# Optimization experiments

Hardware: AMD Instinct MI355X
Metric: run time of the kernel (lower is better)

Reference implementation:

```python
import jax, jax.numpy as jnp
import numpy as np

TOP_K = 2
EPS = 1e-6


def setup_inputs() -> dict:
    key = jax.random.key(0)
    ks = jax.random.split(key, 8)
    B, S, D, E = 4, 2048, 2048, 8
    sd = 1.0 / np.sqrt(D)
    return {
        "x": jax.random.normal(ks[0], (B, S, D), dtype=jnp.float32),
        "Wr": jax.random.normal(ks[1], (D, E), dtype=jnp.float32) * sd,
        "br": jnp.zeros((E,), dtype=jnp.float32),
        "We": jax.random.normal(ks[2], (E, D, D), dtype=jnp.float32) * sd,
        "be": jnp.zeros((E, D), dtype=jnp.float32),
        "Wo": jax.random.normal(ks[3], (D, D), dtype=jnp.float32) * sd,
        "bo": jnp.zeros((D,), dtype=jnp.float32),
        "norm_w": jnp.ones((D,), dtype=jnp.float32),
    }


def reference(x, Wr, br, We, be, Wo, bo, norm_w):
    B, S, D = x.shape
    xf = x.reshape(-1, D)  # [T, D]
    # Router + top-k gating (softmax over the k selected logits, as in source)
    logits = xf @ Wr + br                      # [T, E]
    vals, idx = jax.lax.top_k(logits, TOP_K)   # [T, K]
    gates = jax.nn.softmax(vals, axis=-1)      # [T, K]
    # Expert FFN: Linear -> SiLU (dropout=0 -> identity). Dense over all experts,
    # then gather the top-k outputs per token.
    all_out = jax.nn.silu(jnp.einsum('td,edf->tef', xf, We) + be)  # [T, E, D]
    picked = jnp.take_along_axis(all_out, idx[:, :, None], axis=1)  # [T, K, D]
    combined = jnp.sum(gates[:, :, None] * picked, axis=1)          # [T, D]
    out = combined @ Wo + bo
    y = xf + out
    rms = jnp.sqrt(jnp.mean(y * y, axis=-1, keepdims=True) + EPS)
    return (norm_w * (y / rms)).reshape(B, S, D)
```

## Files before the change

kernel.cpp:

```cpp
#include <hip/hip_runtime.h>
#include <hip/hip_bf16.h>
#include <stdint.h>

typedef __bf16 bf16;
typedef __bf16 bf16x4 __attribute__((ext_vector_type(4)));
typedef __bf16 bf16x8 __attribute__((ext_vector_type(8)));
typedef float floatx4 __attribute__((ext_vector_type(4)));

#define T_TOK 8192
#define DIM 2048
#define NE 8
#define MAX_CHUNKS 136

__device__ inline void gld_lds16(const bf16* g, bf16* l) {
  __builtin_amdgcn_global_load_lds(
      (const __attribute__((address_space(1))) uint32_t*)g,
      (__attribute__((address_space(3))) uint32_t*)l, 16, 0, 0);
}

__global__ __launch_bounds__(256) void transpose_convert(
    const float* __restrict__ in, bf16* __restrict__ out) {
  __shared__ float tile[32][33];
  const int tx = threadIdx.x & 31;
  const int ty = threadIdx.x >> 5;
  const int n0 = blockIdx.x * 32;
  const int k0 = blockIdx.y * 32;
  const size_t base = (size_t)blockIdx.z * DIM * DIM;
  const float* src = in + base;
  bf16* dst = out + base;
#pragma unroll
  for (int i = 0; i < 32; i += 8)
    tile[ty + i][tx] = src[(size_t)(k0 + ty + i) * DIM + n0 + tx];
  __syncthreads();
#pragma unroll
  for (int i = 0; i < 32; i += 8)
    dst[(size_t)(n0 + ty + i) * DIM + k0 + tx] = (bf16)tile[tx][ty + i];
}

__global__ __launch_bounds__(256) void router_kernel(
    const float* __restrict__ x, const float* __restrict__ Wr,
    const float* __restrict__ br, int* __restrict__ cnt,
    int* __restrict__ aid_list, float* __restrict__ gate_list,
    bf16* __restrict__ xb) {
  const int t = blockIdx.x;
  const int tid = threadIdx.x;
  const float* xr = x + (size_t)t * DIM;
  bf16* xbr = xb + (size_t)t * DIM;
  float acc[8];
#pragma unroll
  for (int e = 0; e < 8; ++e) acc[e] = 0.f;
#pragma unroll
  for (int h = 0; h < 2; ++h) {
    const int d0 = tid * 4 + h * 1024;
    float4 xv = *(const float4*)&xr[d0];
    bf16x4 xc;
    xc[0] = (bf16)xv.x; xc[1] = (bf16)xv.y; xc[2] = (bf16)xv.z; xc[3] = (bf16)xv.w;
    *(bf16x4*)&xbr[d0] = xc;
    const float* wp = &Wr[(size_t)d0 * NE];
    float xe[4] = {xv.x, xv.y, xv.z, xv.w};
#pragma unroll
    for (int q = 0; q < 4; ++q) {
      float4 w0 = *(const float4*)&wp[q * 8];
      float4 w1 = *(const float4*)&wp[q * 8 + 4];
      acc[0] += xe[q] * w0.x; acc[1] += xe[q] * w0.y;
      acc[2] += xe[q] * w0.z; acc[3] += xe[q] * w0.w;
      acc[4] += xe[q] * w1.x; acc[5] += xe[q] * w1.y;
      acc[6] += xe[q] * w1.z; acc[7] += xe[q] * w1.w;
    }
  }
#pragma unroll
  for (int e = 0; e < 8; ++e) {
#pragma unroll
    for (int off = 32; off > 0; off >>= 1) acc[e] += __shfl_down(acc[e], off, 64);
  }
  __shared__ float red[4][8];
  const int lane = tid & 63, wid = tid >> 6;
  if (lane == 0) {
#pragma unroll
    for (int e = 0; e < 8; ++e) red[wid][e] = acc[e];
  }
  __syncthreads();
  if (tid == 0) {
    float lg[8];
#pragma unroll
    for (int e = 0; e < 8; ++e)
      lg[e] = red[0][e] + red[1][e] + red[2][e] + red[3][e] + br[e];
    int i0 = 0;
#pragma unroll
    for (int e = 1; e < 8; ++e) if (lg[e] > lg[i0]) i0 = e;
    int i1 = (i0 == 0) ? 1 : 0;
#pragma unroll
    for (int e = 0; e < 8; ++e)
      if (e != i0 && lg[e] > lg[i1]) i1 = e;
    const float g0 = 1.f / (1.f + expf(lg[i1] - lg[i0]));
    const float g1 = 1.f - g0;
    int p0 = atomicAdd(&cnt[i0], 1);
    aid_list[i0 * T_TOK + p0] = t * 2;
    gate_list[i0 * T_TOK + p0] = g0;
    int p1 = atomicAdd(&cnt[i1], 1);
    aid_list[i1 * T_TOK + p1] = t * 2 + 1;
    gate_list[i1 * T_TOK + p1] = g1;
  }
}

__global__ void build_chunks(const int* __restrict__ cnt, int2* __restrict__ chunks,
                             int* __restrict__ nchunks) {
  if (threadIdx.x == 0 && blockIdx.x == 0) {
    int tot = 0;
#pragma unroll
    for (int e = 0; e < NE; ++e) {
      const int ne = cnt[e];
      for (int m0 = 0; m0 < ne; m0 += 128) chunks[tot++] = make_int2(e, m0);
    }
    *nchunks = tot;
  }
}


__global__ __launch_bounds__(256, 2) void expert_gemm(
    const bf16* __restrict__ xb, const bf16* __restrict__ Wt,
    const float* __restrict__ be, const int* __restrict__ cnt,
    const int* __restrict__ aid_list, const float* __restrict__ gate_list,
    const int2* __restrict__ chunks, const int* __restrict__ nchunks,
    bf16* __restrict__ aout) {
  const int cid = blockIdx.x;
  if (cid >= *nchunks) return;
  const int2 ch = chunks[cid];
  const int e = ch.x;
  const int m0 = ch.y;
  const int ne = cnt[e];
  const int n0 = blockIdx.y * 128;
  const int tid = threadIdx.x;

  __shared__ bf16 As[128][64];
  __shared__ bf16 Bs[128][64];
  __shared__ int aidS[128];
  __shared__ float gateS[128];

  if (tid < 128) {
    const int idx = m0 + tid;
    aidS[tid] = (idx < ne) ? aid_list[e * T_TOK + idx] : 0;
    gateS[tid] = (idx < ne) ? gate_list[e * T_TOK + idx] : 0.f;
  }
  __syncthreads();

  const int r0 = tid >> 3;
  const int kq = (((tid & 7) ^ (r0 & 7))) * 8;
  const bf16* wbase = Wt + (size_t)e * DIM * DIM;
  const bf16* ap[4];
  const bf16* bp[4];
#pragma unroll
  for (int h = 0; h < 4; ++h) {
    const int r = r0 + 32 * h;
    ap[h] = xb + (size_t)(aidS[r] >> 1) * DIM + kq;
    bp[h] = wbase + (size_t)(n0 + r) * DIM + kq;
  }
  bf16* const asF = &As[0][0];
  bf16* const bsF = &Bs[0][0];

  const int lane = tid & 63, wid = tid >> 6;
  const int wr = (wid >> 1) * 64, wc = (wid & 1) * 64;
  const int quad = lane >> 4, l15 = lane & 15;

  floatx4 acc[4][4];
#pragma unroll
  for (int i = 0; i < 4; ++i)
#pragma unroll
    for (int j = 0; j < 4; ++j) acc[i][j] = (floatx4){0.f, 0.f, 0.f, 0.f};

  int aoff[2][4], boff[2][4];
#pragma unroll
  for (int s = 0; s < 2; ++s) {
    const int kb = s * 4 + quad;
#pragma unroll
    for (int i = 0; i < 4; ++i) {
      const int mi = wr + i * 16 + l15;
      aoff[s][i] = mi * 64 + ((kb ^ (mi & 7)) * 8);
      const int nj = wc + i * 16 + l15;
      boff[s][i] = nj * 64 + ((kb ^ (nj & 7)) * 8);
    }
  }

  for (int k0 = 0; k0 < DIM; k0 += 64) {
#pragma unroll
    for (int h = 0; h < 4; ++h) {
      gld_lds16(bp[h] + k0, bsF + ((size_t)tid + 256 * h) * 8);
      gld_lds16(ap[h] + k0, asF + ((size_t)tid + 256 * h) * 8);
    }
    __syncthreads();

#pragma unroll
    for (int s = 0; s < 2; ++s) {
      bf16x8 af[4], bfr[4];
#pragma unroll
      for (int i = 0; i < 4; ++i) af[i] = *(const bf16x8*)&asF[aoff[s][i]];
#pragma unroll
      for (int j = 0; j < 4; ++j) bfr[j] = *(const bf16x8*)&bsF[boff[s][j]];
#pragma unroll
      for (int i = 0; i < 4; ++i)
#pragma unroll
        for (int j = 0; j < 4; ++j)
          acc[i][j] = __builtin_amdgcn_mfma_f32_16x16x32_bf16(af[i], bfr[j], acc[i][j], 0, 0, 0);
    }
    __syncthreads();
  }

#pragma unroll
  for (int j = 0; j < 4; ++j) {
    const int col = n0 + wc + j * 16 + l15;
    const float bev = be[e * DIM + col];
#pragma unroll
    for (int i = 0; i < 4; ++i) {
#pragma unroll
      for (int r = 0; r < 4; ++r) {
        const int rl = wr + i * 16 + quad * 4 + r;
        if (m0 + rl < ne) {
          float v = acc[i][j][r] + bev;
          v = v / (1.f + __expf(-v));
          v *= gateS[rl];
          aout[(size_t)aidS[rl] * DIM + col] = (bf16)v;
        }
      }
    }
  }
}

__global__ __launch_bounds__(256) void combine_kernel(
    const bf16* __restrict__ aout, bf16* __restrict__ hcomb) {
  const size_t i = ((size_t)blockIdx.x * 256 + threadIdx.x) * 8;
  const size_t row = i >> 11;
  const size_t d = i & 2047;
  const bf16* a0 = aout + (row << 12) + d;
  bf16x8 u0 = *(const bf16x8*)a0;
  bf16x8 u1 = *(const bf16x8*)(a0 + DIM);
  bf16x8 s;
#pragma unroll
  for (int q = 0; q < 8; ++q) s[q] = (bf16)((float)u0[q] + (float)u1[q]);
  *(bf16x8*)&hcomb[i] = s;
}

__global__ __launch_bounds__(256, 2) void proj_gemm(
    const bf16* __restrict__ hcomb, const bf16* __restrict__ Wot,
    const float* __restrict__ bo, const float* __restrict__ x,
    float* __restrict__ y) {
  const int m0 = blockIdx.x * 128;
  const int n0 = blockIdx.y * 128;
  const int tid = threadIdx.x;

  __shared__ bf16 As[128][64];
  __shared__ bf16 Bs[128][64];

  const int r0 = tid >> 3;
  const int kq = (((tid & 7) ^ (r0 & 7))) * 8;
  const bf16* ap[4];
  const bf16* bp[4];
#pragma unroll
  for (int h = 0; h < 4; ++h) {
    const int r = r0 + 32 * h;
    ap[h] = hcomb + (size_t)(m0 + r) * DIM + kq;
    bp[h] = Wot + (size_t)(n0 + r) * DIM + kq;
  }
  bf16* const asF = &As[0][0];
  bf16* const bsF = &Bs[0][0];

  const int lane = tid & 63, wid = tid >> 6;
  const int wr = (wid >> 1) * 64, wc = (wid & 1) * 64;
  const int quad = lane >> 4, l15 = lane & 15;

  floatx4 acc[4][4];
#pragma unroll
  for (int i = 0; i < 4; ++i)
#pragma unroll
    for (int j = 0; j < 4; ++j) acc[i][j] = (floatx4){0.f, 0.f, 0.f, 0.f};

  int aoff[2][4], boff[2][4];
#pragma unroll
  for (int s = 0; s < 2; ++s) {
    const int kb = s * 4 + quad;
#pragma unroll
    for (int i = 0; i < 4; ++i) {
      const int mi = wr + i * 16 + l15;
      aoff[s][i] = mi * 64 + ((kb ^ (mi & 7)) * 8);
      const int nj = wc + i * 16 + l15;
      boff[s][i] = nj * 64 + ((kb ^ (nj & 7)) * 8);
    }
  }

  for (int k0 = 0; k0 < DIM; k0 += 64) {
#pragma unroll
    for (int h = 0; h < 4; ++h) {
      gld_lds16(bp[h] + k0, bsF + ((size_t)tid + 256 * h) * 8);
      gld_lds16(ap[h] + k0, asF + ((size_t)tid + 256 * h) * 8);
    }
    __syncthreads();

#pragma unroll
    for (int s = 0; s < 2; ++s) {
      bf16x8 af[4], bfr[4];
#pragma unroll
      for (int i = 0; i < 4; ++i) af[i] = *(const bf16x8*)&asF[aoff[s][i]];
#pragma unroll
      for (int j = 0; j < 4; ++j) bfr[j] = *(const bf16x8*)&bsF[boff[s][j]];
#pragma unroll
      for (int i = 0; i < 4; ++i)
#pragma unroll
        for (int j = 0; j < 4; ++j)
          acc[i][j] = __builtin_amdgcn_mfma_f32_16x16x32_bf16(af[i], bfr[j], acc[i][j], 0, 0, 0);
    }
    __syncthreads();
  }

#pragma unroll
  for (int j = 0; j < 4; ++j) {
    const int col = n0 + wc + j * 16 + l15;
    const float bov = bo[col];
#pragma unroll
    for (int i = 0; i < 4; ++i) {
#pragma unroll
      for (int r = 0; r < 4; ++r) {
        const int rl = wr + i * 16 + quad * 4 + r;
        const size_t o = (size_t)(m0 + rl) * DIM + col;
        y[o] = acc[i][j][r] + bov + x[o];
      }
    }
  }
}

__global__ __launch_bounds__(256) void rmsnorm_kernel(
    float* __restrict__ y, const float* __restrict__ w) {
  const int row = blockIdx.x;
  const int tid = threadIdx.x;
  float* yr = y + (size_t)row * DIM;
  float4 v0 = ((const float4*)yr)[tid];
  float4 v1 = ((const float4*)yr)[tid + 256];
  float ss = v0.x * v0.x + v0.y * v0.y + v0.z * v0.z + v0.w * v0.w +
             v1.x * v1.x + v1.y * v1.y + v1.z * v1.z + v1.w * v1.w;
#pragma unroll
  for (int off = 32; off > 0; off >>= 1) ss += __shfl_down(ss, off, 64);
  __shared__ float s4[4];
  const int lane = tid & 63, wid = tid >> 6;
  if (lane == 0) s4[wid] = ss;
  __syncthreads();
  const float tot = s4[0] + s4[1] + s4[2] + s4[3];
  const float r = rsqrtf(tot / (float)DIM + 1e-6f);
  float4 w0 = ((const float4*)w)[tid];
  float4 w1 = ((const float4*)w)[tid + 256];
  float4 o0 = make_float4(v0.x * r * w0.x, v0.y * r * w0.y, v0.z * r * w0.z, v0.w * r * w0.w);
  float4 o1 = make_float4(v1.x * r * w1.x, v1.y * r * w1.y, v1.z * r * w1.z, v1.w * r * w1.w);
  ((float4*)yr)[tid] = o0;
  ((float4*)yr)[tid + 256] = o1;
}

extern "C" void kernel_launch(void* const* d_in, const int* in_sizes, int n_in,
                              void* d_out, int out_size, void* d_ws, size_t ws_size,
                              hipStream_t stream) {
  const float* x  = (const float*)d_in[0];
  const float* Wr = (const float*)d_in[1];
  const float* br = (const float*)d_in[2];
  const float* We = (const float*)d_in[3];
  const float* be = (const float*)d_in[4];
  const float* Wo = (const float*)d_in[5];
  const float* bo = (const float*)d_in[6];
  const float* nw = (const float*)d_in[7];
  float* out = (float*)d_out;

  uint8_t* ws = (uint8_t*)d_ws;
  size_t off = 0;
  auto carve = [&](size_t bytes) -> void* {
    void* p = ws + off;
    off += (bytes + 255) & ~(size_t)255;
    return p;
  };
  int*   cnt       = (int*)carve(NE * sizeof(int));
  int*   aid_list  = (int*)carve((size_t)NE * T_TOK * sizeof(int));
  float* gate_list = (float*)carve((size_t)NE * T_TOK * sizeof(float));
  int2*  chunks    = (int2*)carve(MAX_CHUNKS * sizeof(int2));
  int*   nchunks   = (int*)carve(sizeof(int));
  bf16*  We_t      = (bf16*)carve((size_t)NE * DIM * DIM * sizeof(bf16));
  bf16*  Wo_t      = (bf16*)carve((size_t)DIM * DIM * sizeof(bf16));
  bf16*  aoutb     = (bf16*)carve((size_t)T_TOK * 2 * DIM * sizeof(bf16));
  bf16*  xb        = (bf16*)carve((size_t)T_TOK * DIM * sizeof(bf16));
  bf16*  hcomb     = We_t;
  (void)ws_size; (void)in_sizes; (void)n_in; (void)out_size;

  hipMemsetAsync(cnt, 0, NE * sizeof(int), stream);
  transpose_convert<<<dim3(DIM / 32, DIM / 32, NE), 256, 0, stream>>>(We, We_t);
  transpose_convert<<<dim3(DIM / 32, DIM / 32, 1), 256, 0, stream>>>(Wo, Wo_t);
  router_kernel<<<T_TOK, 256, 0, stream>>>(x, Wr, br, cnt, aid_list, gate_list, xb);
  build_chunks<<<1, 64, 0, stream>>>(cnt, chunks, nchunks);
  expert_gemm<<<dim3(MAX_CHUNKS, DIM / 128), 256, 0, stream>>>(
      xb, We_t, be, cnt, aid_list, gate_list, chunks, nchunks, aoutb);
  combine_kernel<<<(T_TOK * DIM / 8) / 256, 256, 0, stream>>>(aoutb, hcomb);
  proj_gemm<<<dim3(T_TOK / 128, DIM / 128), 256, 0, stream>>>(hcomb, Wo_t, bo, x, out);
  rmsnorm_kernel<<<T_TOK, 256, 0, stream>>>(out, nw);
}
```

Before: 840.6 us.

## Use 256x256 double-buffered GEMM tiles with interleaved prefetch and block swizzle

Expert and projection GEMMs move from 128x128 tiles with 256 threads to 256x256 tiles with 512 threads and a double-buffered LDS. The next K-tile's global-to-LDS loads are spread between the MFMA phases, and setprio is raised around the MFMA bursts. Block indices are remapped so the eight N-column blocks of one M chunk are spread across the grid. The aim is to raise operand reuse, hide load latency and cut barrier stalls, at the cost of 128KB of LDS per block, higher register pressure and coarser padding waste for experts whose token count is not a multiple of 256.

Result: slower. 890.6 us (+6.0%).

```diff
diff --git a/kernel.cpp b/kernel.cpp
--- a/kernel.cpp
+++ b/kernel.cpp
@@ -10,7 +10,9 @@
 #define T_TOK 8192
 #define DIM 2048
 #define NE 8
-#define MAX_CHUNKS 136
+#define NT (DIM / 64)
+#define MAX_CHUNKS 72
+#define PROJ_CIDS 32
 
 __device__ inline void gld_lds16(const bf16* g, bf16* l) {
   __builtin_amdgcn_global_load_lds(
@@ -110,34 +112,70 @@
 #pragma unroll
     for (int e = 0; e < NE; ++e) {
       const int ne = cnt[e];
-      for (int m0 = 0; m0 < ne; m0 += 128) chunks[tot++] = make_int2(e, m0);
+      for (int m0 = 0; m0 < ne; m0 += 256) chunks[tot++] = make_int2(e, m0);
     }
     *nchunks = tot;
   }
 }
 
 
-__global__ __launch_bounds__(256, 2) void expert_gemm(
+#define GEMM_TILE_PHASES(STAGE_EXPR)                                          \
+  {                                                                           \
+    bf16x8 af[4], bfr[4];                                                     \
+_Pragma("unroll")                                                             \
+    for (int s = 0; s < 2; ++s) {                                             \
+      const int xo = s ? x1 : x0;                                             \
+_Pragma("unroll")                                                             \
+      for (int mh = 0; mh < 2; ++mh) {                                        \
+        if (mh == 0) {                                                        \
+_Pragma("unroll")                                                             \
+          for (int j = 0; j < 4; ++j)                                         \
+            bfr[j] = *(const bf16x8*)&bsF[bbase + xo + j * 1024];             \
+        }                                                                     \
+_Pragma("unroll")                                                             \
+        for (int i = 0; i < 4; ++i)                                           \
+          af[i] = *(const bf16x8*)&asF[abase + xo + (mh * 4 + i) * 1024];     \
+        const int ph = s * 2 + mh;                                            \
+        if ((STAGE_EXPR) && ph < 3) {                                         \
+          const int h = ph + 1;                                               \
+          gld_lds16(ap[h] + kn, asN + (size_t)(tid + 512 * h) * 8);           \
+          gld_lds16(bp[h] + kn, bsN + (size_t)(tid + 512 * h) * 8);           \
+        }                                                                     \
+        __builtin_amdgcn_s_setprio(1);                                        \
+_Pragma("unroll")                                                             \
+        for (int i = 0; i < 4; ++i)                                           \
+_Pragma("unroll")                                                             \
+          for (int j = 0; j < 4; ++j)                                         \
+            acc[mh * 4 + i][j] = __builtin_amdgcn_mfma_f32_16x16x32_bf16(     \
+                af[i], bfr[j], acc[mh * 4 + i][j], 0, 0, 0);                  \
+        __builtin_amdgcn_s_setprio(0);                                        \
+      }                                                                       \
+    }                                                                         \
+  }
+
+__global__ __launch_bounds__(512, 2) void expert_gemm(
     const bf16* __restrict__ xb, const bf16* __restrict__ Wt,
     const float* __restrict__ be, const int* __restrict__ cnt,
     const int* __restrict__ aid_list, const float* __restrict__ gate_list,
     const int2* __restrict__ chunks, const int* __restrict__ nchunks,
     bf16* __restrict__ aout) {
-  const int cid = blockIdx.x;
+  int wg = blockIdx.x;
+  wg = (wg & 7) * MAX_CHUNKS + (wg >> 3);
+  const int cid = wg >> 3;
   if (cid >= *nchunks) return;
   const int2 ch = chunks[cid];
   const int e = ch.x;
   const int m0 = ch.y;
   const int ne = cnt[e];
-  const int n0 = blockIdx.y * 128;
+  const int n0 = (wg & 7) * 256;
   const int tid = threadIdx.x;
 
-  __shared__ bf16 As[128][64];
-  __shared__ bf16 Bs[128][64];
-  __shared__ int aidS[128];
-  __shared__ float gateS[128];
-
-  if (tid < 128) {
+  __shared__ bf16 As[2][256 * 64];
+  __shared__ bf16 Bs[2][256 * 64];
+  __shared__ int aidS[256];
+  __shared__ float gateS[256];
+
+  if (tid < 256) {
     const int idx = m0 + tid;
     aidS[tid] = (idx < ne) ? aid_list[e * T_TOK + idx] : 0;
     gateS[tid] = (idx < ne) ? gate_list[e * T_TOK + idx] : 0.f;
@@ -145,75 +183,71 @@
   __syncthreads();
 
   const int r0 = tid >> 3;
-  const int kq = (((tid & 7) ^ (r0 & 7))) * 8;
+  const int kq = ((tid & 7) ^ (r0 & 7)) * 8;
   const bf16* wbase = Wt + (size_t)e * DIM * DIM;
   const bf16* ap[4];
   const bf16* bp[4];
 #pragma unroll
   for (int h = 0; h < 4; ++h) {
-    const int r = r0 + 32 * h;
+    const int r = r0 + 64 * h;
     ap[h] = xb + (size_t)(aidS[r] >> 1) * DIM + kq;
     bp[h] = wbase + (size_t)(n0 + r) * DIM + kq;
   }
-  bf16* const asF = &As[0][0];
-  bf16* const bsF = &Bs[0][0];
-
-  const int lane = tid & 63, wid = tid >> 6;
-  const int wr = (wid >> 1) * 64, wc = (wid & 1) * 64;
+
+  const int lane = tid & 63, w = tid >> 6;
+  const int wm = w >> 2, wn = w & 3;
   const int quad = lane >> 4, l15 = lane & 15;
-
-  floatx4 acc[4][4];
-#pragma unroll
-  for (int i = 0; i < 4; ++i)
+  const int x0 = ((quad) ^ (l15 & 7)) * 8;
+  const int x1 = ((quad + 4) ^ (l15 & 7)) * 8;
+  const int abase = (wm * 128 + l15) * 64;
+  const int bbase = (wn * 64 + l15) * 64;
+
+  floatx4 acc[8][4];
+#pragma unroll
+  for (int i = 0; i < 8; ++i)
 #pragma unroll
     for (int j = 0; j < 4; ++j) acc[i][j] = (floatx4){0.f, 0.f, 0.f, 0.f};
 
-  int aoff[2][4], boff[2][4];
-#pragma unroll
-  for (int s = 0; s < 2; ++s) {
-    const int kb = s * 4 + quad;
-#pragma unroll
-    for (int i = 0; i < 4; ++i) {
-      const int mi = wr + i * 16 + l15;
-      aoff[s][i] = mi * 64 + ((kb ^ (mi & 7)) * 8);
-      const int nj = wc + i * 16 + l15;
-      boff[s][i] = nj * 64 + ((kb ^ (nj & 7)) * 8);
-    }
-  }
-
-  for (int k0 = 0; k0 < DIM; k0 += 64) {
-#pragma unroll
-    for (int h = 0; h < 4; ++h) {
-      gld_lds16(bp[h] + k0, bsF + ((size_t)tid + 256 * h) * 8);
-      gld_lds16(ap[h] + k0, asF + ((size_t)tid + 256 * h) * 8);
-    }
-    __syncthreads();
-
-#pragma unroll
-    for (int s = 0; s < 2; ++s) {
-      bf16x8 af[4], bfr[4];
-#pragma unroll
-      for (int i = 0; i < 4; ++i) af[i] = *(const bf16x8*)&asF[aoff[s][i]];
-#pragma unroll
-      for (int j = 0; j < 4; ++j) bfr[j] = *(const bf16x8*)&bsF[boff[s][j]];
-#pragma unroll
-      for (int i = 0; i < 4; ++i)
-#pragma unroll
-        for (int j = 0; j < 4; ++j)
-          acc[i][j] = __builtin_amdgcn_mfma_f32_16x16x32_bf16(af[i], bfr[j], acc[i][j], 0, 0, 0);
-    }
-    __syncthreads();
+#pragma unroll
+  for (int h = 0; h < 4; ++h) {
+    gld_lds16(ap[h], &As[0][(size_t)(tid + 512 * h) * 8]);
+    gld_lds16(bp[h], &Bs[0][(size_t)(tid + 512 * h) * 8]);
+  }
+
+  int p = 0;
+  for (int t = 0; t < NT; ++t) {
+    const bf16* asF = &As[p][0];
+    const bf16* bsF = &Bs[p][0];
+    bf16* asN = &As[p ^ 1][0];
+    bf16* bsN = &Bs[p ^ 1][0];
+    const int kn = (t + 1) * 64;
+    const bool stage = (t + 1 < NT);
+
+    asm volatile("" ::: "memory");
+    __builtin_amdgcn_s_barrier();
+    if (stage) {
+      gld_lds16(ap[0] + kn, asN + (size_t)tid * 8);
+      gld_lds16(bp[0] + kn, bsN + (size_t)tid * 8);
+      asm volatile("s_waitcnt vmcnt(2)" ::: "memory");
+    } else {
+      asm volatile("s_waitcnt vmcnt(0)" ::: "memory");
+    }
+    __builtin_amdgcn_s_barrier();
+    asm volatile("" ::: "memory");
+
+    GEMM_TILE_PHASES(stage)
+    p ^= 1;
   }
 
 #pragma unroll
   for (int j = 0; j < 4; ++j) {
-    const int col = n0 + wc + j * 16 + l15;
+    const int col = n0 + wn * 64 + j * 16 + l15;
     const float bev = be[e * DIM + col];
 #pragma unroll
-    for (int i = 0; i < 4; ++i) {
+    for (int i = 0; i < 8; ++i) {
 #pragma unroll
       for (int r = 0; r < 4; ++r) {
-        const int rl = wr + i * 16 + quad * 4 + r;
+        const int rl = wm * 128 + i * 16 + quad * 4 + r;
         if (m0 + rl < ne) {
           float v = acc[i][j][r] + bev;
           v = v / (1.f + __expf(-v));
@@ -239,86 +273,84 @@
   *(bf16x8*)&hcomb[i] = s;
 }
 
-__global__ __launch_bounds__(256, 2) void proj_gemm(
+__global__ __launch_bounds__(512, 2) void proj_gemm(
     const bf16* __restrict__ hcomb, const bf16* __restrict__ Wot,
     const float* __restrict__ bo, const float* __restrict__ x,
     float* __restrict__ y) {
-  const int m0 = blockIdx.x * 128;
-  const int n0 = blockIdx.y * 128;
+  int wg = blockIdx.x;
+  wg = (wg & 7) * PROJ_CIDS + (wg >> 3);
+  const int m0 = (wg >> 3) * 256;
+  const int n0 = (wg & 7) * 256;
   const int tid = threadIdx.x;
 
-  __shared__ bf16 As[128][64];
-  __shared__ bf16 Bs[128][64];
+  __shared__ bf16 As[2][256 * 64];
+  __shared__ bf16 Bs[2][256 * 64];
 
   const int r0 = tid >> 3;
-  const int kq = (((tid & 7) ^ (r0 & 7))) * 8;
+  const int kq = ((tid & 7) ^ (r0 & 7)) * 8;
   const bf16* ap[4];
   const bf16* bp[4];
 #pragma unroll
   for (int h = 0; h < 4; ++h) {
-    const int r = r0 + 32 * h;
+    const int r = r0 + 64 * h;
     ap[h] = hcomb + (size_t)(m0 + r) * DIM + kq;
     bp[h] = Wot + (size_t)(n0 + r) * DIM + kq;
   }
-  bf16* const asF = &As[0][0];
-  bf16* const bsF = &Bs[0][0];
-
-  const int lane = tid & 63, wid = tid >> 6;
-  const int wr = (wid >> 1) * 64, wc = (wid & 1) * 64;
+
+  const int lane = tid & 63, w = tid >> 6;
+  const int wm = w >> 2, wn = w & 3;
   const int quad = lane >> 4, l15 = lane & 15;
-
-  floatx4 acc[4][4];
-#pragma unroll
-  for (int i = 0; i < 4; ++i)
+  const int x0 = ((quad) ^ (l15 & 7)) * 8;
+  const int x1 = ((quad + 4) ^ (l15 & 7)) * 8;
+  const int abase = (wm * 128 + l15) * 64;
+  const int bbase = (wn * 64 + l15) * 64;
+
+  floatx4 acc[8][4];
+#pragma unroll
+  for (int i = 0; i < 8; ++i)
 #pragma unroll
     for (int j = 0; j < 4; ++j) acc[i][j] = (floatx4){0.f, 0.f, 0.f, 0.f};
 
-  int aoff[2][4], boff[2][4];
-#pragma unroll
-  for (int s = 0; s < 2; ++s) {
-    const int kb = s * 4 + quad;
-#pragma unroll
-    for (int i = 0; i < 4; ++i) {
-      const int mi = wr + i * 16 + l15;
-      aoff[s][i] = mi * 64 + ((kb ^ (mi & 7)) * 8);
-      const int nj = wc + i * 16 + l15;
-      boff[s][i] = nj * 64 + ((kb ^ (nj & 7)) * 8);
-    }
-  }
-
-  for (int k0 = 0; k0 < DIM; k0 += 64) {
-#pragma unroll
-    for (int h = 0; h < 4; ++h) {
-      gld_lds16(bp[h] + k0, bsF + ((size_t)tid + 256 * h) * 8);
-      gld_lds16(ap[h] + k0, asF + ((size_t)tid + 256 * h) * 8);
-    }
-    __syncthreads();
-
-#pragma unroll
-    for (int s = 0; s < 2; ++s) {
-      bf16x8 af[4], bfr[4];
-#pragma unroll
-      for (int i = 0; i < 4; ++i) af[i] = *(const bf16x8*)&asF[aoff[s][i]];
-#pragma unroll
-      for (int j = 0; j < 4; ++j) bfr[j] = *(const bf16x8*)&bsF[boff[s][j]];
-#pragma unroll
-      for (int i = 0; i < 4; ++i)
-#pragma unroll
-        for (int j = 0; j < 4; ++j)
-          acc[i][j] = __builtin_amdgcn_mfma_f32_16x16x32_bf16(af[i], bfr[j], acc[i][j], 0, 0, 0);
-    }
-    __syncthreads();
+#pragma unroll
+  for (int h = 0; h < 4; ++h) {
+    gld_lds16(ap[h], &As[0][(size_t)(tid + 512 * h) * 8]);
+    gld_lds16(bp[h], &Bs[0][(size_t)(tid + 512 * h) * 8]);
+  }
+
+  int p = 0;
+  for (int t = 0; t < NT; ++t) {
+    const bf16* asF = &As[p][0];
+    const bf16* bsF = &Bs[p][0];
+    bf16* asN = &As[p ^ 1][0];
+    bf16* bsN = &Bs[p ^ 1][0];
+    const int kn = (t + 1) * 64;
+    const bool stage = (t + 1 < NT);
+
+    asm volatile("" ::: "memory");
+    __builtin_amdgcn_s_barrier();
+    if (stage) {
+      gld_lds16(ap[0] + kn, asN + (size_t)tid * 8);
+      gld_lds16(bp[0] + kn, bsN + (size_t)tid * 8);
+      asm volatile("s_waitcnt vmcnt(2)" ::: "memory");
+    } else {
+      asm volatile("s_waitcnt vmcnt(0)" ::: "memory");
+    }
+    __builtin_amdgcn_s_barrier();
+    asm volatile("" ::: "memory");
+
+    GEMM_TILE_PHASES(stage)
+    p ^= 1;
   }
 
 #pragma unroll
   for (int j = 0; j < 4; ++j) {
-    const int col = n0 + wc + j * 16 + l15;
+    const int col = n0 + wn * 64 + j * 16 + l15;
     const float bov = bo[col];
 #pragma unroll
-    for (int i = 0; i < 4; ++i) {
+    for (int i = 0; i < 8; ++i) {
 #pragma unroll
       for (int r = 0; r < 4; ++r) {
-        const int rl = wr + i * 16 + quad * 4 + r;
+        const int rl = wm * 128 + i * 16 + quad * 4 + r;
         const size_t o = (size_t)(m0 + rl) * DIM + col;
         y[o] = acc[i][j][r] + bov + x[o];
       }
@@ -388,9 +420,9 @@
   transpose_convert<<<dim3(DIM / 32, DIM / 32, 1), 256, 0, stream>>>(Wo, Wo_t);
   router_kernel<<<T_TOK, 256, 0, stream>>>(x, Wr, br, cnt, aid_list, gate_list, xb);
   build_chunks<<<1, 64, 0, stream>>>(cnt, chunks, nchunks);
-  expert_gemm<<<dim3(MAX_CHUNKS, DIM / 128), 256, 0, stream>>>(
+  expert_gemm<<<dim3(MAX_CHUNKS * 8), 512, 0, stream>>>(
       xb, We_t, be, cnt, aid_list, gate_list, chunks, nchunks, aoutb);
   combine_kernel<<<(T_TOK * DIM / 8) / 256, 256, 0, stream>>>(aoutb, hcomb);
-  proj_gemm<<<dim3(T_TOK / 128, DIM / 128), 256, 0, stream>>>(hcomb, Wo_t, bo, x, out);
+  proj_gemm<<<dim3(PROJ_CIDS * 8), 512, 0, stream>>>(hcomb, Wo_t, bo, x, out);
   rmsnorm_kernel<<<T_TOK, 256, 0, stream>>>(out, nw);
 }
```

## Double-buffer GEMM K-loop and fuse top-2 combine into projection A-load

Applied to the files above, without the earlier changes.

Both expert and projection GEMMs switch to BK=32 double-buffered LDS tiles, prefetching the next tile while MFMAs run on the current one, with occupancy hint raised to 4 blocks per CU. The separate combine kernel is removed; proj_gemm now loads both per-token expert outputs, sums them in registers and writes the sum to LDS, saving a full intermediate write/read pass. Grids are flattened to 1D with N-tiles fastest, so consecutive blocks share the same A rows. Trade-offs are twice as many barriers per K and register-path A loads in proj_gemm instead of direct-to-LDS loads.

New measurement: 863.8 us. 1.03x slower.

```diff
diff --git a/kernel.cpp b/kernel.cpp
--- a/kernel.cpp
+++ b/kernel.cpp
@@ -10,6 +10,10 @@
 #define T_TOK 8192
 #define DIM 2048
 #define NE 8
+#define BM 128
+#define BN 128
+#define BK 32
+#define NTIL (DIM / BK)
 #define MAX_CHUNKS 136
 
 __device__ inline void gld_lds16(const bf16* g, bf16* l) {
@@ -110,57 +114,62 @@
 #pragma unroll
     for (int e = 0; e < NE; ++e) {
       const int ne = cnt[e];
-      for (int m0 = 0; m0 < ne; m0 += 128) chunks[tot++] = make_int2(e, m0);
+      for (int m0 = 0; m0 < ne; m0 += BM) chunks[tot++] = make_int2(e, m0);
     }
     *nchunks = tot;
   }
 }
 
 
-__global__ __launch_bounds__(256, 2) void expert_gemm(
+__global__ __launch_bounds__(256, 4) void expert_gemm(
     const bf16* __restrict__ xb, const bf16* __restrict__ Wt,
     const float* __restrict__ be, const int* __restrict__ cnt,
     const int* __restrict__ aid_list, const float* __restrict__ gate_list,
     const int2* __restrict__ chunks, const int* __restrict__ nchunks,
     bf16* __restrict__ aout) {
-  const int cid = blockIdx.x;
+  const int cid = blockIdx.x >> 4;
   if (cid >= *nchunks) return;
   const int2 ch = chunks[cid];
   const int e = ch.x;
   const int m0 = ch.y;
   const int ne = cnt[e];
-  const int n0 = blockIdx.y * 128;
+  const int n0 = (blockIdx.x & 15) * BN;
   const int tid = threadIdx.x;
 
-  __shared__ bf16 As[128][64];
-  __shared__ bf16 Bs[128][64];
-  __shared__ int aidS[128];
-  __shared__ float gateS[128];
-
-  if (tid < 128) {
+  __shared__ bf16 As[2][BM * BK];
+  __shared__ bf16 Bs[2][BM * BK];
+  __shared__ int aidS[BM];
+  __shared__ float gateS[BM];
+
+  if (tid < BM) {
     const int idx = m0 + tid;
     aidS[tid] = (idx < ne) ? aid_list[e * T_TOK + idx] : 0;
     gateS[tid] = (idx < ne) ? gate_list[e * T_TOK + idx] : 0.f;
   }
   __syncthreads();
 
-  const int r0 = tid >> 3;
-  const int kq = (((tid & 7) ^ (r0 & 7))) * 8;
-  const bf16* wbase = Wt + (size_t)e * DIM * DIM;
-  const bf16* ap[4];
-  const bf16* bp[4];
-#pragma unroll
-  for (int h = 0; h < 4; ++h) {
-    const int r = r0 + 32 * h;
+  const int kq = ((tid & 3) ^ ((tid >> 3) & 3)) * 8;
+  const int r0 = tid >> 2;
+  const bf16* wb = Wt + (size_t)e * DIM * DIM;
+  const bf16* ap[2];
+  const bf16* bp[2];
+#pragma unroll
+  for (int h = 0; h < 2; ++h) {
+    const int r = r0 + 64 * h;
     ap[h] = xb + (size_t)(aidS[r] >> 1) * DIM + kq;
-    bp[h] = wbase + (size_t)(n0 + r) * DIM + kq;
-  }
-  bf16* const asF = &As[0][0];
-  bf16* const bsF = &Bs[0][0];
-
-  const int lane = tid & 63, wid = tid >> 6;
-  const int wr = (wid >> 1) * 64, wc = (wid & 1) * 64;
+    bp[h] = wb + (size_t)(n0 + r) * DIM + kq;
+  }
+
+  const int lane = tid & 63, w = tid >> 6;
+  const int wm = w >> 1, wn = w & 1;
   const int quad = lane >> 4, l15 = lane & 15;
+  const int xo = (quad ^ ((l15 >> 1) & 3)) * 8;
+  int aoff[4], boff[4];
+#pragma unroll
+  for (int i = 0; i < 4; ++i) {
+    aoff[i] = (wm * 64 + i * 16 + l15) * BK + xo;
+    boff[i] = (wn * 64 + i * 16 + l15) * BK + xo;
+  }
 
   floatx4 acc[4][4];
 #pragma unroll
@@ -168,52 +177,51 @@
 #pragma unroll
     for (int j = 0; j < 4; ++j) acc[i][j] = (floatx4){0.f, 0.f, 0.f, 0.f};
 
-  int aoff[2][4], boff[2][4];
-#pragma unroll
-  for (int s = 0; s < 2; ++s) {
-    const int kb = s * 4 + quad;
+  bf16* a_cur = &As[0][0]; bf16* a_nxt = &As[1][0];
+  bf16* b_cur = &Bs[0][0]; bf16* b_nxt = &Bs[1][0];
+
+#pragma unroll
+  for (int h = 0; h < 2; ++h) {
+    gld_lds16(ap[h], a_cur + (tid + 256 * h) * 8);
+    gld_lds16(bp[h], b_cur + (tid + 256 * h) * 8);
+  }
+  asm volatile("s_waitcnt vmcnt(0)" ::: "memory");
+  __builtin_amdgcn_s_barrier();
+
+  for (int t = 0; t < NTIL; ++t) {
+    if (t + 1 < NTIL) {
+      const int kn = (t + 1) * BK;
+#pragma unroll
+      for (int h = 0; h < 2; ++h) {
+        gld_lds16(ap[h] + kn, a_nxt + (tid + 256 * h) * 8);
+        gld_lds16(bp[h] + kn, b_nxt + (tid + 256 * h) * 8);
+      }
+    }
+    bf16x8 af[4];
+#pragma unroll
+    for (int i = 0; i < 4; ++i) af[i] = *(const bf16x8*)&a_cur[aoff[i]];
+#pragma unroll
+    for (int j = 0; j < 4; ++j) {
+      const bf16x8 bfr = *(const bf16x8*)&b_cur[boff[j]];
+#pragma unroll
+      for (int i = 0; i < 4; ++i)
+        acc[i][j] = __builtin_amdgcn_mfma_f32_16x16x32_bf16(af[i], bfr, acc[i][j], 0, 0, 0);
+    }
+    asm volatile("s_waitcnt vmcnt(0)" ::: "memory");
+    __builtin_amdgcn_s_barrier();
+    bf16* tA = a_cur; a_cur = a_nxt; a_nxt = tA;
+    bf16* tB = b_cur; b_cur = b_nxt; b_nxt = tB;
+  }
+
+#pragma unroll
+  for (int j = 0; j < 4; ++j) {
+    const int col = n0 + wn * 64 + j * 16 + l15;
+    const float bev = be[e * DIM + col];
 #pragma unroll
     for (int i = 0; i < 4; ++i) {
-      const int mi = wr + i * 16 + l15;
-      aoff[s][i] = mi * 64 + ((kb ^ (mi & 7)) * 8);
-      const int nj = wc + i * 16 + l15;
-      boff[s][i] = nj * 64 + ((kb ^ (nj & 7)) * 8);
-    }
-  }
-
-  for (int k0 = 0; k0 < DIM; k0 += 64) {
-#pragma unroll
-    for (int h = 0; h < 4; ++h) {
-      gld_lds16(bp[h] + k0, bsF + ((size_t)tid + 256 * h) * 8);
-      gld_lds16(ap[h] + k0, asF + ((size_t)tid + 256 * h) * 8);
-    }
-    __syncthreads();
-
-#pragma unroll
-    for (int s = 0; s < 2; ++s) {
-      bf16x8 af[4], bfr[4];
-#pragma unroll
-      for (int i = 0; i < 4; ++i) af[i] = *(const bf16x8*)&asF[aoff[s][i]];
-#pragma unroll
-      for (int j = 0; j < 4; ++j) bfr[j] = *(const bf16x8*)&bsF[boff[s][j]];
-#pragma unroll
-      for (int i = 0; i < 4; ++i)
-#pragma unroll
-        for (int j = 0; j < 4; ++j)
-          acc[i][j] = __builtin_amdgcn_mfma_f32_16x16x32_bf16(af[i], bfr[j], acc[i][j], 0, 0, 0);
-    }
-    __syncthreads();
-  }
-
-#pragma unroll
-  for (int j = 0; j < 4; ++j) {
-    const int col = n0 + wc + j * 16 + l15;
-    const float bev = be[e * DIM + col];
-#pragma unroll
-    for (int i = 0; i < 4; ++i) {
 #pragma unroll
       for (int r = 0; r < 4; ++r) {
-        const int rl = wr + i * 16 + quad * 4 + r;
+        const int rl = wm * 64 + i * 16 + quad * 4 + r;
         if (m0 + rl < ne) {
           float v = acc[i][j][r] + bev;
           v = v / (1.f + __expf(-v));
@@ -225,47 +233,38 @@
   }
 }
 
-__global__ __launch_bounds__(256) void combine_kernel(
-    const bf16* __restrict__ aout, bf16* __restrict__ hcomb) {
-  const size_t i = ((size_t)blockIdx.x * 256 + threadIdx.x) * 8;
-  const size_t row = i >> 11;
-  const size_t d = i & 2047;
-  const bf16* a0 = aout + (row << 12) + d;
-  bf16x8 u0 = *(const bf16x8*)a0;
-  bf16x8 u1 = *(const bf16x8*)(a0 + DIM);
-  bf16x8 s;
-#pragma unroll
-  for (int q = 0; q < 8; ++q) s[q] = (bf16)((float)u0[q] + (float)u1[q]);
-  *(bf16x8*)&hcomb[i] = s;
-}
-
-__global__ __launch_bounds__(256, 2) void proj_gemm(
-    const bf16* __restrict__ hcomb, const bf16* __restrict__ Wot,
+__global__ __launch_bounds__(256, 4) void proj_gemm(
+    const bf16* __restrict__ aout, const bf16* __restrict__ Wot,
     const float* __restrict__ bo, const float* __restrict__ x,
     float* __restrict__ y) {
-  const int m0 = blockIdx.x * 128;
-  const int n0 = blockIdx.y * 128;
+  const int m0 = (int)(blockIdx.x >> 4) * BM;
+  const int n0 = (int)(blockIdx.x & 15) * BN;
   const int tid = threadIdx.x;
 
-  __shared__ bf16 As[128][64];
-  __shared__ bf16 Bs[128][64];
-
-  const int r0 = tid >> 3;
-  const int kq = (((tid & 7) ^ (r0 & 7))) * 8;
-  const bf16* ap[4];
-  const bf16* bp[4];
-#pragma unroll
-  for (int h = 0; h < 4; ++h) {
-    const int r = r0 + 32 * h;
-    ap[h] = hcomb + (size_t)(m0 + r) * DIM + kq;
+  __shared__ bf16 As[2][BM * BK];
+  __shared__ bf16 Bs[2][BM * BK];
+
+  const int kq = ((tid & 3) ^ ((tid >> 3) & 3)) * 8;
+  const int r0 = tid >> 2;
+  const bf16* a0[2];
+  const bf16* bp[2];
+#pragma unroll
+  for (int h = 0; h < 2; ++h) {
+    const int r = r0 + 64 * h;
+    a0[h] = aout + (size_t)(2 * (m0 + r)) * DIM + kq;
     bp[h] = Wot + (size_t)(n0 + r) * DIM + kq;
   }
-  bf16* const asF = &As[0][0];
-  bf16* const bsF = &Bs[0][0];
-
-  const int lane = tid & 63, wid = tid >> 6;
-  const int wr = (wid >> 1) * 64, wc = (wid & 1) * 64;
+
+  const int lane = tid & 63, w = tid >> 6;
+  const int wm = w >> 1, wn = w & 1;
   const int quad = lane >> 4, l15 = lane & 15;
+  const int xo = (quad ^ ((l15 >> 1) & 3)) * 8;
+  int aoff[4], boff[4];
+#pragma unroll
+  for (int i = 0; i < 4; ++i) {
+    aoff[i] = (wm * 64 + i * 16 + l15) * BK + xo;
+    boff[i] = (wn * 64 + i * 16 + l15) * BK + xo;
+  }
 
   floatx4 acc[4][4];
 #pragma unroll
@@ -273,52 +272,76 @@
 #pragma unroll
     for (int j = 0; j < 4; ++j) acc[i][j] = (floatx4){0.f, 0.f, 0.f, 0.f};
 
-  int aoff[2][4], boff[2][4];
-#pragma unroll
-  for (int s = 0; s < 2; ++s) {
-    const int kb = s * 4 + quad;
+  bf16* a_cur = &As[0][0]; bf16* a_nxt = &As[1][0];
+  bf16* b_cur = &Bs[0][0]; bf16* b_nxt = &Bs[1][0];
+
+  {
+    bf16x8 u[2][2];
+#pragma unroll
+    for (int h = 0; h < 2; ++h) {
+      gld_lds16(bp[h], b_cur + (tid + 256 * h) * 8);
+      u[h][0] = *(const bf16x8*)(a0[h]);
+      u[h][1] = *(const bf16x8*)(a0[h] + DIM);
+    }
+#pragma unroll
+    for (int h = 0; h < 2; ++h) {
+      bf16x8 s;
+#pragma unroll
+      for (int q = 0; q < 8; ++q)
+        s[q] = (bf16)((float)u[h][0][q] + (float)u[h][1][q]);
+      *(bf16x8*)&a_cur[(tid + 256 * h) * 8] = s;
+    }
+  }
+  asm volatile("s_waitcnt vmcnt(0) lgkmcnt(0)" ::: "memory");
+  __builtin_amdgcn_s_barrier();
+
+  for (int t = 0; t < NTIL; ++t) {
+    bf16x8 v[2][2];
+    const bool stage = (t + 1 < NTIL);
+    if (stage) {
+      const int kn = (t + 1) * BK;
+#pragma unroll
+      for (int h = 0; h < 2; ++h) {
+        gld_lds16(bp[h] + kn, b_nxt + (tid + 256 * h) * 8);
+        v[h][0] = *(const bf16x8*)(a0[h] + kn);
+        v[h][1] = *(const bf16x8*)(a0[h] + kn + DIM);
+      }
+    }
+    bf16x8 af[4];
+#pragma unroll
+    for (int i = 0; i < 4; ++i) af[i] = *(const bf16x8*)&a_cur[aoff[i]];
+#pragma unroll
+    for (int j = 0; j < 4; ++j) {
+      const bf16x8 bfr = *(const bf16x8*)&b_cur[boff[j]];
+#pragma unroll
+      for (int i = 0; i < 4; ++i)
+        acc[i][j] = __builtin_amdgcn_mfma_f32_16x16x32_bf16(af[i], bfr, acc[i][j], 0, 0, 0);
+    }
+    if (stage) {
+#pragma unroll
+      for (int h = 0; h < 2; ++h) {
+        bf16x8 s;
+#pragma unroll
+        for (int q = 0; q < 8; ++q)
+          s[q] = (bf16)((float)v[h][0][q] + (float)v[h][1][q]);
+        *(bf16x8*)&a_nxt[(tid + 256 * h) * 8] = s;
+      }
+    }
+    asm volatile("s_waitcnt vmcnt(0) lgkmcnt(0)" ::: "memory");
+    __builtin_amdgcn_s_barrier();
+    bf16* tA = a_cur; a_cur = a_nxt; a_nxt = tA;
+    bf16* tB = b_cur; b_cur = b_nxt; b_nxt = tB;
+  }
+
+#pragma unroll
+  for (int j = 0; j < 4; ++j) {
+    const int col = n0 + wn * 64 + j * 16 + l15;
+    const float bov = bo[col];
 #pragma unroll
     for (int i = 0; i < 4; ++i) {
-      const int mi = wr + i * 16 + l15;
-      aoff[s][i] = mi * 64 + ((kb ^ (mi & 7)) * 8);
-      const int nj = wc + i * 16 + l15;
-      boff[s][i] = nj * 64 + ((kb ^ (nj & 7)) * 8);
-    }
-  }
-
-  for (int k0 = 0; k0 < DIM; k0 += 64) {
-#pragma unroll
-    for (int h = 0; h < 4; ++h) {
-      gld_lds16(bp[h] + k0, bsF + ((size_t)tid + 256 * h) * 8);
-      gld_lds16(ap[h] + k0, asF + ((size_t)tid + 256 * h) * 8);
-    }
-    __syncthreads();
-
-#pragma unroll
-    for (int s = 0; s < 2; ++s) {
-      bf16x8 af[4], bfr[4];
-#pragma unroll
-      for (int i = 0; i < 4; ++i) af[i] = *(const bf16x8*)&asF[aoff[s][i]];
-#pragma unroll
-      for (int j = 0; j < 4; ++j) bfr[j] = *(const bf16x8*)&bsF[boff[s][j]];
-#pragma unroll
-      for (int i = 0; i < 4; ++i)
-#pragma unroll
-        for (int j = 0; j < 4; ++j)
-          acc[i][j] = __builtin_amdgcn_mfma_f32_16x16x32_bf16(af[i], bfr[j], acc[i][j], 0, 0, 0);
-    }
-    __syncthreads();
-  }
-
-#pragma unroll
-  for (int j = 0; j < 4; ++j) {
-    const int col = n0 + wc + j * 16 + l15;
-    const float bov = bo[col];
-#pragma unroll
-    for (int i = 0; i < 4; ++i) {
 #pragma unroll
       for (int r = 0; r < 4; ++r) {
-        const int rl = wr + i * 16 + quad * 4 + r;
+        const int rl = wm * 64 + i * 16 + quad * 4 + r;
         const size_t o = (size_t)(m0 + rl) * DIM + col;
         y[o] = acc[i][j][r] + bov + x[o];
       }
@@ -380,7 +403,6 @@
   bf16*  Wo_t      = (bf16*)carve((size_t)DIM * DIM * sizeof(bf16));
   bf16*  aoutb     = (bf16*)carve((size_t)T_TOK * 2 * DIM * sizeof(bf16));
   bf16*  xb        = (bf16*)carve((size_t)T_TOK * DIM * sizeof(bf16));
-  bf16*  hcomb     = We_t;
   (void)ws_size; (void)in_sizes; (void)n_in; (void)out_size;
 
   hipMemsetAsync(cnt, 0, NE * sizeof(int), stream);
@@ -388,9 +410,8 @@
   transpose_convert<<<dim3(DIM / 32, DIM / 32, 1), 256, 0, stream>>>(Wo, Wo_t);
   router_kernel<<<T_TOK, 256, 0, stream>>>(x, Wr, br, cnt, aid_list, gate_list, xb);
   build_chunks<<<1, 64, 0, stream>>>(cnt, chunks, nchunks);
-  expert_gemm<<<dim3(MAX_CHUNKS, DIM / 128), 256, 0, stream>>>(
+  expert_gemm<<<dim3(MAX_CHUNKS * 16), 256, 0, stream>>>(
       xb, We_t, be, cnt, aid_list, gate_list, chunks, nchunks, aoutb);
-  combine_kernel<<<(T_TOK * DIM / 8) / 256, 256, 0, stream>>>(aoutb, hcomb);
-  proj_gemm<<<dim3(T_TOK / 128, DIM / 128), 256, 0, stream>>>(hcomb, Wo_t, bo, x, out);
+  proj_gemm<<<dim3((T_TOK / BM) * 16), 256, 0, stream>>>(aoutb, Wo_t, bo, x, out);
   rmsnorm_kernel<<<T_TOK, 256, 0, stream>>>(out, nw);
 }
```

## Scatter tokens into expert-grouped buffers and fuse combine into projection GEMM

Applied to the files above, without the earlier changes.

The router now writes each token's bf16 copy directly into per-expert padded row buffers and records an inverse index. The expert GEMM therefore reads contiguous A rows and writes contiguous outputs. The separate combine kernel is removed: the projection GEMM gathers both expert outputs per token through registers, sums them, and stores them to shared memory. Chunk building is computed inline, the cnt memset and the two transposes are merged into one launch, and launch bounds go to 3 blocks per SM. The risks are a per-expert count above EPAD overflowing its buffer, and the loss of the direct global-to-LDS load for the projection A operand.

Result: no change. 853.8 us (+1.6%).

```diff
diff --git a/kernel.cpp b/kernel.cpp
--- a/kernel.cpp
+++ b/kernel.cpp
@@ -10,6 +10,7 @@
 #define T_TOK 8192
 #define DIM 2048
 #define NE 8
+#define EPAD 2560
 #define MAX_CHUNKS 136
 
 __device__ inline void gld_lds16(const bf16* g, bf16* l) {
@@ -19,15 +20,18 @@
 }
 
 __global__ __launch_bounds__(256) void transpose_convert(
-    const float* __restrict__ in, bf16* __restrict__ out) {
+    const float* __restrict__ We, const float* __restrict__ Wo,
+    bf16* __restrict__ We_t, bf16* __restrict__ Wo_t, int* __restrict__ cnt) {
+  const int z = blockIdx.z;
+  if (z == 8 && blockIdx.x == 0 && blockIdx.y == 0 && threadIdx.x < NE)
+    cnt[threadIdx.x] = 0;
+  const float* src = (z < 8) ? We + (size_t)z * DIM * DIM : Wo;
+  bf16* dst = (z < 8) ? We_t + (size_t)z * DIM * DIM : Wo_t;
   __shared__ float tile[32][33];
   const int tx = threadIdx.x & 31;
   const int ty = threadIdx.x >> 5;
   const int n0 = blockIdx.x * 32;
   const int k0 = blockIdx.y * 32;
-  const size_t base = (size_t)blockIdx.z * DIM * DIM;
-  const float* src = in + base;
-  bf16* dst = out + base;
 #pragma unroll
   for (int i = 0; i < 32; i += 8)
     tile[ty + i][tx] = src[(size_t)(k0 + ty + i) * DIM + n0 + tx];
@@ -40,24 +44,21 @@
 __global__ __launch_bounds__(256) void router_kernel(
     const float* __restrict__ x, const float* __restrict__ Wr,
     const float* __restrict__ br, int* __restrict__ cnt,
-    int* __restrict__ aid_list, float* __restrict__ gate_list,
-    bf16* __restrict__ xb) {
+    float* __restrict__ gate_list, int2* __restrict__ inv,
+    bf16* __restrict__ xg) {
   const int t = blockIdx.x;
   const int tid = threadIdx.x;
   const float* xr = x + (size_t)t * DIM;
-  bf16* xbr = xb + (size_t)t * DIM;
+  float4 xv[2];
   float acc[8];
 #pragma unroll
   for (int e = 0; e < 8; ++e) acc[e] = 0.f;
 #pragma unroll
   for (int h = 0; h < 2; ++h) {
     const int d0 = tid * 4 + h * 1024;
-    float4 xv = *(const float4*)&xr[d0];
-    bf16x4 xc;
-    xc[0] = (bf16)xv.x; xc[1] = (bf16)xv.y; xc[2] = (bf16)xv.z; xc[3] = (bf16)xv.w;
-    *(bf16x4*)&xbr[d0] = xc;
+    xv[h] = *(const float4*)&xr[d0];
     const float* wp = &Wr[(size_t)d0 * NE];
-    float xe[4] = {xv.x, xv.y, xv.z, xv.w};
+    float xe[4] = {xv[h].x, xv[h].y, xv[h].z, xv[h].w};
 #pragma unroll
     for (int q = 0; q < 4; ++q) {
       float4 w0 = *(const float4*)&wp[q * 8];
@@ -74,6 +75,7 @@
     for (int off = 32; off > 0; off >>= 1) acc[e] += __shfl_down(acc[e], off, 64);
   }
   __shared__ float red[4][8];
+  __shared__ int sRow[2];
   const int lane = tid & 63, wid = tid >> 6;
   if (lane == 0) {
 #pragma unroll
@@ -94,72 +96,73 @@
       if (e != i0 && lg[e] > lg[i1]) i1 = e;
     const float g0 = 1.f / (1.f + expf(lg[i1] - lg[i0]));
     const float g1 = 1.f - g0;
-    int p0 = atomicAdd(&cnt[i0], 1);
-    aid_list[i0 * T_TOK + p0] = t * 2;
+    const int p0 = atomicAdd(&cnt[i0], 1);
+    const int p1 = atomicAdd(&cnt[i1], 1);
     gate_list[i0 * T_TOK + p0] = g0;
-    int p1 = atomicAdd(&cnt[i1], 1);
-    aid_list[i1 * T_TOK + p1] = t * 2 + 1;
     gate_list[i1 * T_TOK + p1] = g1;
-  }
-}
-
-__global__ void build_chunks(const int* __restrict__ cnt, int2* __restrict__ chunks,
-                             int* __restrict__ nchunks) {
-  if (threadIdx.x == 0 && blockIdx.x == 0) {
-    int tot = 0;
-#pragma unroll
-    for (int e = 0; e < NE; ++e) {
-      const int ne = cnt[e];
-      for (int m0 = 0; m0 < ne; m0 += 128) chunks[tot++] = make_int2(e, m0);
-    }
-    *nchunks = tot;
-  }
-}
-
-
-__global__ __launch_bounds__(256, 2) void expert_gemm(
-    const bf16* __restrict__ xb, const bf16* __restrict__ Wt,
+    sRow[0] = i0 * EPAD + p0;
+    sRow[1] = i1 * EPAD + p1;
+    inv[t] = make_int2(sRow[0], sRow[1]);
+  }
+  __syncthreads();
+  const size_t r0 = (size_t)sRow[0] * DIM;
+  const size_t r1 = (size_t)sRow[1] * DIM;
+#pragma unroll
+  for (int h = 0; h < 2; ++h) {
+    const int d0 = tid * 4 + h * 1024;
+    bf16x4 xc;
+    xc[0] = (bf16)xv[h].x; xc[1] = (bf16)xv[h].y;
+    xc[2] = (bf16)xv[h].z; xc[3] = (bf16)xv[h].w;
+    *(bf16x4*)&xg[r0 + d0] = xc;
+    *(bf16x4*)&xg[r1 + d0] = xc;
+  }
+}
+
+
+__global__ __launch_bounds__(256, 3) void expert_gemm(
+    const bf16* __restrict__ xg, const bf16* __restrict__ Wt,
     const float* __restrict__ be, const int* __restrict__ cnt,
-    const int* __restrict__ aid_list, const float* __restrict__ gate_list,
-    const int2* __restrict__ chunks, const int* __restrict__ nchunks,
-    bf16* __restrict__ aout) {
+    const float* __restrict__ gate_list, bf16* __restrict__ aoutc) {
   const int cid = blockIdx.x;
-  if (cid >= *nchunks) return;
-  const int2 ch = chunks[cid];
-  const int e = ch.x;
-  const int m0 = ch.y;
+  int e = -1, m0 = 0;
+  {
+    int acc = 0;
+#pragma unroll
+    for (int q = 0; q < NE; ++q) {
+      const int c = (cnt[q] + 127) >> 7;
+      if (e < 0 && cid < acc + c) { e = q; m0 = (cid - acc) * 128; }
+      acc += c;
+    }
+  }
+  if (e < 0) return;
   const int ne = cnt[e];
   const int n0 = blockIdx.y * 128;
   const int tid = threadIdx.x;
 
-  __shared__ bf16 As[128][64];
-  __shared__ bf16 Bs[128][64];
-  __shared__ int aidS[128];
+  __shared__ bf16 As[128 * 64];
+  __shared__ bf16 Bs[128 * 64];
   __shared__ float gateS[128];
 
-  if (tid < 128) {
-    const int idx = m0 + tid;
-    aidS[tid] = (idx < ne) ? aid_list[e * T_TOK + idx] : 0;
-    gateS[tid] = (idx < ne) ? gate_list[e * T_TOK + idx] : 0.f;
-  }
-  __syncthreads();
+  if (tid < 128)
+    gateS[tid] = (m0 + tid < ne) ? gate_list[e * T_TOK + m0 + tid] : 0.f;
 
   const int r0 = tid >> 3;
-  const int kq = (((tid & 7) ^ (r0 & 7))) * 8;
+  const int kq = ((tid & 7) ^ (r0 & 7)) * 8;
   const bf16* wbase = Wt + (size_t)e * DIM * DIM;
+  const bf16* abase = xg + (size_t)(e * EPAD + m0) * DIM;
   const bf16* ap[4];
   const bf16* bp[4];
 #pragma unroll
   for (int h = 0; h < 4; ++h) {
     const int r = r0 + 32 * h;
-    ap[h] = xb + (size_t)(aidS[r] >> 1) * DIM + kq;
+    ap[h] = abase + (size_t)r * DIM + kq;
     bp[h] = wbase + (size_t)(n0 + r) * DIM + kq;
   }
-  bf16* const asF = &As[0][0];
-  bf16* const bsF = &Bs[0][0];
-
-  const int lane = tid & 63, wid = tid >> 6;
-  const int wr = (wid >> 1) * 64, wc = (wid & 1) * 64;
+  bf16* const asF = As;
+  bf16* const bsF = Bs;
+
+  const int lane = tid & 63, w = tid >> 6;
+  const int wr = (w >> 1) * 64, wc = (w & 1) * 64;
   const int quad = lane >> 4, l15 = lane & 15;
 
   floatx4 acc[4][4];
@@ -188,7 +191,6 @@
       gld_lds16(ap[h] + k0, asF + ((size_t)tid + 256 * h) * 8);
     }
     __syncthreads();
-
 #pragma unroll
     for (int s = 0; s < 2; ++s) {
       bf16x8 af[4], bfr[4];
@@ -218,53 +220,42 @@
           float v = acc[i][j][r] + bev;
           v = v / (1.f + __expf(-v));
           v *= gateS[rl];
-          aout[(size_t)aidS[rl] * DIM + col] = (bf16)v;
+          aoutc[(size_t)(e * EPAD + m0 + rl) * DIM + col] = (bf16)v;
         }
       }
     }
   }
 }
 
-__global__ __launch_bounds__(256) void combine_kernel(
-    const bf16* __restrict__ aout, bf16* __restrict__ hcomb) {
-  const size_t i = ((size_t)blockIdx.x * 256 + threadIdx.x) * 8;
-  const size_t row = i >> 11;
-  const size_t d = i & 2047;
-  const bf16* a0 = aout + (row << 12) + d;
-  bf16x8 u0 = *(const bf16x8*)a0;
-  bf16x8 u1 = *(const bf16x8*)(a0 + DIM);
-  bf16x8 s;
-#pragma unroll
-  for (int q = 0; q < 8; ++q) s[q] = (bf16)((float)u0[q] + (float)u1[q]);
-  *(bf16x8*)&hcomb[i] = s;
-}
-
-__global__ __launch_bounds__(256, 2) void proj_gemm(
-    const bf16* __restrict__ hcomb, const bf16* __restrict__ Wot,
-    const float* __restrict__ bo, const float* __restrict__ x,
-    float* __restrict__ y) {
+__global__ __launch_bounds__(256, 3) void proj_gemm(
+    const bf16* __restrict__ aoutc, const bf16* __restrict__ Wot,
+    const int2* __restrict__ inv, const float* __restrict__ bo,
+    const float* __restrict__ x, float* __restrict__ y) {
   const int m0 = blockIdx.x * 128;
   const int n0 = blockIdx.y * 128;
   const int tid = threadIdx.x;
 
-  __shared__ bf16 As[128][64];
-  __shared__ bf16 Bs[128][64];
+  __shared__ bf16 As[128 * 64];
+  __shared__ bf16 Bs[128 * 64];
 
   const int r0 = tid >> 3;
-  const int kq = (((tid & 7) ^ (r0 & 7))) * 8;
-  const bf16* ap[4];
+  const int kq = ((tid & 7) ^ (r0 & 7)) * 8;
+  const bf16* a0[4];
+  const bf16* a1[4];
   const bf16* bp[4];
 #pragma unroll
   for (int h = 0; h < 4; ++h) {
     const int r = r0 + 32 * h;
-    ap[h] = hcomb + (size_t)(m0 + r) * DIM + kq;
+    const int2 iv = inv[m0 + r];
+    a0[h] = aoutc + (size_t)iv.x * DIM + kq;
+    a1[h] = aoutc + (size_t)iv.y * DIM + kq;
     bp[h] = Wot + (size_t)(n0 + r) * DIM + kq;
   }
-  bf16* const asF = &As[0][0];
-  bf16* const bsF = &Bs[0][0];
-
-  const int lane = tid & 63, wid = tid >> 6;
-  const int wr = (wid >> 1) * 64, wc = (wid & 1) * 64;
+  bf16* const asF = As;
+  bf16* const bsF = Bs;
+
+  const int lane = tid & 63, w = tid >> 6;
+  const int wr = (w >> 1) * 64, wc = (w & 1) * 64;
   const int quad = lane >> 4, l15 = lane & 15;
 
   floatx4 acc[4][4];
@@ -288,12 +279,23 @@
 
   for (int k0 = 0; k0 < DIM; k0 += 64) {
 #pragma unroll
+    for (int h = 0; h < 4; ++h)
+      gld_lds16(bp[h] + k0, bsF + ((size_t)tid + 256 * h) * 8);
+    bf16x8 u0[4], u1[4];
+#pragma unroll
     for (int h = 0; h < 4; ++h) {
-      gld_lds16(bp[h] + k0, bsF + ((size_t)tid + 256 * h) * 8);
-      gld_lds16(ap[h] + k0, asF + ((size_t)tid + 256 * h) * 8);
+      u0[h] = *(const bf16x8*)(a0[h] + k0);
+      u1[h] = *(const bf16x8*)(a1[h] + k0);
+    }
+#pragma unroll
+    for (int h = 0; h < 4; ++h) {
+      bf16x8 s;
+#pragma unroll
+      for (int q = 0; q < 8; ++q)
+        s[q] = (bf16)((float)u0[h][q] + (float)u1[h][q]);
+      *(bf16x8*)&asF[((size_t)tid + 256 * h) * 8] = s;
     }
     __syncthreads();
-
 #pragma unroll
     for (int s = 0; s < 2; ++s) {
       bf16x8 af[4], bfr[4];
@@ -372,25 +374,20 @@
     return p;
   };
   int*   cnt       = (int*)carve(NE * sizeof(int));
-  int*   aid_list  = (int*)carve((size_t)NE * T_TOK * sizeof(int));
   float* gate_list = (float*)carve((size_t)NE * T_TOK * sizeof(float));
-  int2*  chunks    = (int2*)carve(MAX_CHUNKS * sizeof(int2));
-  int*   nchunks   = (int*)carve(sizeof(int));
+  int2*  inv       = (int2*)carve((size_t)T_TOK * sizeof(int2));
   bf16*  We_t      = (bf16*)carve((size_t)NE * DIM * DIM * sizeof(bf16));
   bf16*  Wo_t      = (bf16*)carve((size_t)DIM * DIM * sizeof(bf16));
-  bf16*  aoutb     = (bf16*)carve((size_t)T_TOK * 2 * DIM * sizeof(bf16));
-  bf16*  xb        = (bf16*)carve((size_t)T_TOK * DIM * sizeof(bf16));
-  bf16*  hcomb     = We_t;
+  bf16*  xg        = (bf16*)carve((size_t)NE * EPAD * DIM * sizeof(bf16));
+  bf16*  aoutc     = (bf16*)carve((size_t)NE * EPAD * DIM * sizeof(bf16));
   (void)ws_size; (void)in_sizes; (void)n_in; (void)out_size;
 
-  hipMemsetAsync(cnt, 0, NE * sizeof(int), stream);
-  transpose_convert<<<dim3(DIM / 32, DIM / 32, NE), 256, 0, stream>>>(We, We_t);
-  transpose_convert<<<dim3(DIM / 32, DIM / 32, 1), 256, 0, stream>>>(Wo, Wo_t);
-  router_kernel<<<T_TOK, 256, 0, stream>>>(x, Wr, br, cnt, aid_list, gate_list, xb);
-  build_chunks<<<1, 64, 0, stream>>>(cnt, chunks, nchunks);
+  transpose_convert<<<dim3(DIM / 32, DIM / 32, NE + 1), 256, 0, stream>>>(
+      We, Wo, We_t, Wo_t, cnt);
+  router_kernel<<<T_TOK, 256, 0, stream>>>(x, Wr, br, cnt, gate_list, inv, xg);
   expert_gemm<<<dim3(MAX_CHUNKS, DIM / 128), 256, 0, stream>>>(
-      xb, We_t, be, cnt, aid_list, gate_list, chunks, nchunks, aoutb);
-  combine_kernel<<<(T_TOK * DIM / 8) / 256, 256, 0, stream>>>(aoutb, hcomb);
-  proj_gemm<<<dim3(T_TOK / 128, DIM / 128), 256, 0, stream>>>(hcomb, Wo_t, bo, x, out);
+      xg, We_t, be, cnt, gate_list, aoutc);
+  proj_gemm<<<dim3(T_TOK / 128, DIM / 128), 256, 0, stream>>>(
+      aoutc, Wo_t, inv, bo, x, out);
   rmsnorm_kernel<<<T_TOK, 256, 0, stream>>>(out, nw);
 }
```
